# Kernel optimization log

Measured on AMD Instinct MI355X. Metric: run time of the kernel, lower is better.

## Reference

```python
import jax, jax.numpy as jnp
from jax import lax
import numpy as np

HH = WW = 128          # backbone feature map (2048px image / stride 16)
C_IN = 512
FEAT_STRIDE = 16
N_ANCHOR = 9
NMS_THRESH = 0.7
N_PRE_NMS = 6000
N_POST_NMS = 300
MIN_SIZE = 16
NEG = jnp.float32(-1e30)


def _anchor_base(base_size=16, ratios=(0.5, 1.0, 2.0), scales=(8, 16, 32)):
    py = px = base_size / 2.0
    ab = np.zeros((len(ratios) * len(scales), 4), np.float32)
    for i, r in enumerate(ratios):
        for j, s in enumerate(scales):
            h = base_size * s * np.sqrt(r)
            w = base_size * s * np.sqrt(1.0 / r)
            ab[i * len(scales) + j] = [py - h / 2, px - w / 2, py + h / 2, px + w / 2]
    return ab


def _shifted_anchors(hh, ww):
    # (y1, x1, y2, x2) anchors enumerated row-major over (y, x), anchors innermost
    ab = _anchor_base()
    sy = np.arange(0, hh * FEAT_STRIDE, FEAT_STRIDE, dtype=np.float32)
    sx = np.arange(0, ww * FEAT_STRIDE, FEAT_STRIDE, dtype=np.float32)
    sx, sy = np.meshgrid(sx, sy)
    shift = np.stack((sy.ravel(), sx.ravel(), sy.ravel(), sx.ravel()), axis=1)
    anc = (ab[None, :, :] + shift[:, None, :]).reshape(-1, 4)
    return jnp.asarray(anc)


def _conv(x, w, b):
    y = lax.conv_general_dilated(x, w, (1, 1), 'SAME',
                                 dimension_numbers=('NHWC', 'HWIO', 'NHWC'))
    return y + b


def _loc2bbox(anchor, loc):
    sh = anchor[:, 2] - anchor[:, 0]
    sw = anchor[:, 3] - anchor[:, 1]
    scy = anchor[:, 0] + 0.5 * sh
    scx = anchor[:, 1] + 0.5 * sw
    cy = loc[:, 0] * sh + scy
    cx = loc[:, 1] * sw + scx
    h = jnp.exp(loc[:, 2]) * sh
    w = jnp.exp(loc[:, 3]) * sw
    return jnp.stack([cy - 0.5 * h, cx - 0.5 * w, cy + 0.5 * h, cx + 0.5 * w], axis=1)


def _nms(boxes, scores, thresh, n_out):
    # Greedy NMS with a fixed output size; invalid slots are zeroed.
    y1, x1, y2, x2 = boxes[:, 0], boxes[:, 1], boxes[:, 2], boxes[:, 3]
    areas = (y2 - y1) * (x2 - x1)

    def step(valid, _):
        s = jnp.where(valid, scores, NEG)
        i = jnp.argmax(s)
        ok = s[i] > NEG
        iy1 = jnp.maximum(y1, y1[i]); ix1 = jnp.maximum(x1, x1[i])
        iy2 = jnp.minimum(y2, y2[i]); ix2 = jnp.minimum(x2, x2[i])
        inter = jnp.maximum(iy2 - iy1, 0.0) * jnp.maximum(ix2 - ix1, 0.0)
        iou = inter / (areas + areas[i] - inter + 1e-9)
        valid = valid & (iou <= thresh)  # picked box suppresses itself (iou=1)
        return valid, (i, ok)

    _, (idx, oks) = lax.scan(step, jnp.ones(scores.shape, bool), None, length=n_out)
    return boxes[idx] * oks[:, None].astype(boxes.dtype)


def _proposals(loc, fg_score, anchor, img_h, img_w, scale):
    dst = _loc2bbox(anchor, loc)
    dst = jnp.stack([jnp.clip(dst[:, 0], 0.0, img_h),
                     jnp.clip(dst[:, 1], 0.0, img_w),
                     jnp.clip(dst[:, 2], 0.0, img_h),
                     jnp.clip(dst[:, 3], 0.0, img_w)], axis=1)
    min_size = MIN_SIZE * scale
    hs = dst[:, 2] - dst[:, 0]
    ws = dst[:, 3] - dst[:, 1]
    keep = (hs >= min_size) & (ws >= min_size)
    sc = jnp.where(keep, fg_score, -jnp.inf)
    top_s, top_i = lax.top_k(sc, N_PRE_NMS)
    return _nms(dst[top_i], top_s, NMS_THRESH, N_POST_NMS)


def _rpn_forward(x, conv_w, conv_b, loc_w, loc_b, score_w, score_b, img_h, img_w, scale):
    n, hh, ww, _ = x.shape
    anchor = _shifted_anchors(hh, ww)                    # [hh*ww*9, 4]
    h = jax.nn.relu(_conv(x, conv_w, conv_b))            # [n, hh, ww, 512]
    rpn_loc = _conv(h, loc_w, loc_b).reshape(n, -1, 4)   # [n, hh*ww*9, 4]
    rpn_score_map = _conv(h, score_w, score_b)           # [n, hh, ww, 18]
    soft = jax.nn.softmax(rpn_score_map.reshape(n, hh, ww, N_ANCHOR, 2), axis=-1)
    rpn_fg = soft[..., 1].reshape(n, -1)                 # [n, hh*ww*9]
    rpn_score = rpn_score_map.reshape(n, -1, 2)
    roi = _proposals(rpn_loc[0], rpn_fg[0], anchor, img_h, img_w, scale)  # [300, 4]
    return rpn_loc, rpn_score, roi, anchor


def setup_inputs() -> dict:
    key = jax.random.key(0)
    ks = jax.random.split(key, 4)
    return {
        "x": jax.random.normal(ks[0], (1, HH, WW, C_IN), jnp.float32),
        "conv_w": jax.random.normal(ks[1], (3, 3, C_IN, 512), jnp.float32) * 0.02,
        "conv_b": jnp.zeros((512,), jnp.float32),
        "loc_w": jax.random.normal(ks[2], (1, 1, 512, 36), jnp.float32) * 0.02,
        "loc_b": jnp.zeros((36,), jnp.float32),
        "score_w": jax.random.normal(ks[3], (1, 1, 512, 18), jnp.float32) * 0.02,
        "score_b": jnp.zeros((18,), jnp.float32),
        "img_h": HH * FEAT_STRIDE,
        "img_w": WW * FEAT_STRIDE,
        "scale": 1,
    }


def reference(x, conv_w, conv_b, loc_w, loc_b, score_w, score_b, img_h, img_w, scale):
    return _rpn_forward(x, conv_w, conv_b, loc_w, loc_b, score_w, score_b,
                        float(img_h), float(img_w), float(scale))
```

## Files before the change

### kernel.cpp

```cpp
#include <hip/hip_runtime.h>
#include <math.h>

typedef unsigned int u32;
typedef unsigned long long u64;
typedef _Float16 half8 __attribute__((ext_vector_type(8)));
typedef float f32x4 __attribute__((ext_vector_type(4)));
typedef float f32x16 __attribute__((ext_vector_type(16)));

#define N_PIX 16384
#define N_ANC 147456
#define N_PRE 6000
#define TIE_BASE 6144
#define TIE_CAP  16384

#define OFF_H      0ULL
#define OFF_BOXES  33554432ULL
#define OFF_KEYS   35913728ULL
#define OFF_W54    36503552ULL
#define OFF_B54    36634624ULL
#define OFF_HIST1  36634880ULL
#define OFF_HIST2  36897024ULL
#define OFF_CTRL   37159168ULL
#define OFF_CAND   37159424ULL
#define OFF_SBOX   37339648ULL
#define OFF_MASK   37437952ULL
#define BASE_NEEDED 41961984ULL
#define OFF_XH     41961984ULL
#define OFF_XL     58739200ULL
#define OFF_WHT    75516416ULL
#define OFF_WLT    80235008ULL
#define FULL_NEEDED 84953600ULL

#define KEY_NEGINF 0x007FFFFFu

#define MASK_BYTES 4524032ULL

struct AB { float v[36]; };


__device__ __forceinline__ void d_init_body(int i0, u32* hist1, u32* hist2, u32* ctrl, float* roi,
                       float* w54, float* b54,
                       const float* __restrict__ loc_w, const float* __restrict__ loc_b,
                       const float* __restrict__ score_w, const float* __restrict__ score_b) {
  const int stride = 256 * 256;
  const int TOT = 65536 * 2 + 64 + 1200 + 32768 + 64;
  for (int i = i0; i < TOT; i += stride) {
    if (i < 65536) hist1[i] = 0u;
    else if (i < 131072) hist2[i - 65536] = 0u;
    else if (i < 131136) ctrl[i - 131072] = 0u;
    else if (i < 132336) roi[i - 131136] = 0.f;
    else if (i < 165104) {
      int j = i - 132336;
      int k = j >> 6, oc = j & 63;
      float v = 0.f;
      if (oc < 36) v = loc_w[k * 36 + oc];
      else if (oc < 54) v = score_w[k * 18 + oc - 36];
      w54[(((k >> 2) << 6) + oc) * 4 + (k & 3)] = v;
    } else {
      int oc = i - 165104;
      float v = 0.f;
      if (oc < 36) v = loc_b[oc];
      else if (oc < 54) v = score_b[oc - 36];
      b54[oc] = v;
    }
  }
}

__device__ __forceinline__ void d_split_x_body(int b, int t, const float* __restrict__ x,
                                               _Float16* __restrict__ xh, _Float16* __restrict__ xl) {
  const int gid = b * 256 + t;
  const int base = gid << 3;
  float a[8];
  *(float4*)&a[0] = *(const float4*)(x + base);
  *(float4*)&a[4] = *(const float4*)(x + base + 4);
  half8 hh, ll;
#pragma unroll
  for (int j = 0; j < 8; ++j) {
    _Float16 hi = (_Float16)a[j];
    hh[j] = hi;
    ll[j] = (_Float16)((a[j] - (float)hi) * 2048.0f);
  }
  *(half8*)(xh + base) = hh;
  *(half8*)(xl + base) = ll;
}

__device__ __forceinline__ void d_split_w_body(int kb64, int ob, int t, const float* __restrict__ w,
                                               _Float16* __restrict__ whPK, _Float16* __restrict__ wlPK,
                                               _Float16 (*th)[72], _Float16 (*tl)[72]) {
  {
    const int r = t >> 2, cq = t & 3;
    float a[16];
    const float* wp = w + ((size_t)(kb64 * 64 + r) << 9) + ob * 64 + cq * 16;
#pragma unroll
    for (int j = 0; j < 4; ++j) *(float4*)&a[j << 2] = *(const float4*)(wp + (j << 2));
    half8 h0, h1, l0, l1;
#pragma unroll
    for (int j = 0; j < 8; ++j) {
      _Float16 hi = (_Float16)a[j];
      h0[j] = hi; l0[j] = (_Float16)((a[j] - (float)hi) * 2048.0f);
    }
#pragma unroll
    for (int j = 0; j < 8; ++j) {
      _Float16 hi = (_Float16)a[8 + j];
      h1[j] = hi; l1[j] = (_Float16)((a[8 + j] - (float)hi) * 2048.0f);
    }
    *(half8*)&th[r][cq * 16]     = h0;
    *(half8*)&th[r][cq * 16 + 8] = h1;
    *(half8*)&tl[r][cq * 16]     = l0;
    *(half8*)&tl[r][cq * 16 + 8] = l1;
  }
  __syncthreads();
  {
    const int o_local = t & 63;
    const int hl = (t >> 6) & 1;
    const int cs = t >> 7;
    const int tap = kb64 >> 3;
    const int ci  = ((kb64 & 7) << 1) + cs;
    const int kb  = ci * 9 + tap;
    const int o   = ob * 64 + o_local;
    const int nb  = o >> 7, n = o & 127;
    _Float16* dst = (hl ? wlPK : whPK) + (((size_t)(nb * 144 + kb)) << 12) + n * 8;
    _Float16 (*src)[72] = hl ? tl : th;
    const int r0 = cs << 5;
#pragma unroll
    for (int q = 0; q < 4; ++q) {
      half8 v;
#pragma unroll
      for (int j = 0; j < 8; ++j) v[j] = src[r0 + (q << 3) + j][o_local];
      *(half8*)(dst + (q << 10)) = v;
    }
  }
}

__global__ void k_init(u32* hist1, u32* hist2, u32* ctrl, float* roi,
                       float* w54, float* b54,
                       const float* __restrict__ loc_w, const float* __restrict__ loc_b,
                       const float* __restrict__ score_w, const float* __restrict__ score_b) {
  const int i0 = blockIdx.x * blockDim.x + threadIdx.x;
  d_init_body(i0, hist1, hist2, ctrl, roi, w54, b54, loc_w, loc_b, score_w, score_b);
}

__global__ __launch_bounds__(256) void k_prep(const float* __restrict__ x,
                                              _Float16* __restrict__ xh, _Float16* __restrict__ xl,
                                              const float* __restrict__ w,
                                              _Float16* __restrict__ whPK, _Float16* __restrict__ wlPK,
                                              u32* hist1, u32* hist2, u32* ctrl, float* roi,
                                              float* w54, float* b54,
                                              const float* __restrict__ loc_w, const float* __restrict__ loc_b,
                                              const float* __restrict__ score_w, const float* __restrict__ score_b) {
  __shared__ _Float16 th[64][72];
  __shared__ _Float16 tl[64][72];
  const int b = blockIdx.x;
  const int t = threadIdx.x;
  if (b < 4096) {
    d_split_x_body(b, t, x, xh, xl);
  } else if (b < 4672) {
    const int idx = b - 4096;
    d_split_w_body(idx % 72, idx / 72, t, w, whPK, wlPK, th, tl);
  } else {
    d_init_body((b - 4672) * 256 + t, hist1, hist2, ctrl, roi, w54, b54, loc_w, loc_b, score_w, score_b);
  }
}

__global__ __launch_bounds__(256, 2) void k_conv_pre(const _Float16* __restrict__ xh,
                                                     const _Float16* __restrict__ xl,
                                                     const _Float16* __restrict__ whPK,
                                                     const _Float16* __restrict__ wlPK,
                                                     const float* __restrict__ bias,
                                                     float* __restrict__ h) {
  __shared__ _Float16 As[2][2][4][128][8];

  const int bid = blockIdx.x;
  const int q   = bid >> 3;
  const int nb  = q >> 4;
  const int y   = ((bid & 7) << 4) + (q & 15);

  const int t  = threadIdx.x;
  const int wv = t >> 6, lane = t & 63;
  const int m0 = (wv >> 1) << 6;
  const int n0 = (wv & 1) << 6;
  const int ln5 = lane & 31;
  const int kh  = lane >> 5;

  const int s_m = t >> 1;
  const int kq0 = (t & 1) << 1;
  const int ch0 = kq0 << 3;

  f32x16 acc_hh[2][2];
  f32x16 acc_x[2][2];
#pragma unroll
  for (int i = 0; i < 2; ++i)
#pragma unroll
    for (int j = 0; j < 2; ++j) { acc_hh[i][j] = (f32x16)0.f; acc_x[i][j] = (f32x16)0.f; }

  const int ct0 = (s_m - 1) << 9;
  const int ct1 = s_m << 9;
  const int ct2 = (s_m + 1) << 9;
  const bool cok0 = (s_m >= 1);
  const bool cok2 = (s_m <= 126);

  const u32 wb = ((u32)kh << 10) + (((u32)(n0 + ln5)) << 3);

  half8 rah0, rah1, ral0, ral1;
  half8 bh0[2][2], bl0[2][2], bh1[2][2], bl1[2][2];

#define CONV_LOADA(KB)                                                           \
  {                                                                              \
    const int ci_   = (KB) / 9;                                                  \
    const int tap_  = (KB) - ci_ * 9;                                            \
    const int ky_   = tap_ / 3, kx_ = tap_ - ky_ * 3;                            \
    const int cin0_ = ci_ << 5;                                                  \
    const int yy_   = y + ky_ - 1;                                               \
    const bool rok_ = (yy_ >= 0) && (yy_ < 128);                                 \
    const int colterm_ = (kx_ == 0) ? ct0 : ((kx_ == 1) ? ct1 : ct2);            \
    const bool cok_    = (kx_ == 0) ? cok0 : ((kx_ == 1) ? true : cok2);         \
    if (rok_ && cok_) {                                                          \
      const u32 aoff_ = (u32)((yy_ << 16) + cin0_ + ch0 + colterm_);             \
      rah0 = *(const half8*)(xh + aoff_);                                        \
      rah1 = *(const half8*)(xh + aoff_ + 8);                                    \
      ral0 = *(const half8*)(xl + aoff_);                                        \
      ral1 = *(const half8*)(xl + aoff_ + 8);                                    \
    } else {                                                                     \
      rah0 = (half8)(_Float16)0; rah1 = (half8)(_Float16)0;                      \
      ral0 = (half8)(_Float16)0; ral1 = (half8)(_Float16)0;                      \
    }                                                                            \
  }

#define CONV_STOREA(BUF)                                                         \
  {                                                                              \
    *(half8*)As[BUF][0][kq0][s_m]     = rah0;                                    \
    *(half8*)As[BUF][0][kq0 + 1][s_m] = rah1;                                    \
    *(half8*)As[BUF][1][kq0][s_m]     = ral0;                                    \
    *(half8*)As[BUF][1][kq0 + 1][s_m] = ral1;                                    \
  }

#define BLOAD(KB, BH, BL)                                                        \
  {                                                                              \
    const u32 kbase_ = ((u32)(nb * 144 + (KB))) << 12;    \
    _Pragma("unroll")                                                            \
    for (int i_ = 0; i_ < 2; ++i_) {                                             \
      _Pragma("unroll")                                                          \
      for (int ks_ = 0; ks_ < 2; ++ks_) {                                        \
        const u32 o_ = kbase_ + ((u32)ks_ << 11) + wb + ((u32)i_ << 8);          \
        BH[i_][ks_] = *(const half8*)(whPK + o_);                                \
        BL[i_][ks_] = *(const half8*)(wlPK + o_);                                \
      }                                                                          \
    }                                                                            \
  }

#define FRAGSA(KS, AH, AL)                                                       \
  {                                                                              \
    const int kq_ = ((KS) << 1) + kh;                                            \
    _Pragma("unroll")                                                            \
    for (int i = 0; i < 2; ++i) {                                                \
      AH[i] = *(const half8*)As[cur][0][kq_][m0 + (i << 5) + ln5];               \
      AL[i] = *(const half8*)As[cur][1][kq_][m0 + (i << 5) + ln5];               \
    }                                                                            \
  }

#define MFMA6(AH, AL, BH, BL, KS)                                                \
  {                                                                              \
    _Pragma("unroll")                                                            \
    for (int mi = 0; mi < 2; ++mi)                                               \
      _Pragma("unroll")                                                          \
      for (int ni = 0; ni < 2; ++ni) {                                           \
        acc_hh[mi][ni] = __builtin_amdgcn_mfma_f32_32x32x16_f16(AH[mi], BH[ni][KS], acc_hh[mi][ni], 0, 0, 0); \
        acc_x[mi][ni]  = __builtin_amdgcn_mfma_f32_32x32x16_f16(AH[mi], BL[ni][KS], acc_x[mi][ni], 0, 0, 0);  \
        acc_x[mi][ni]  = __builtin_amdgcn_mfma_f32_32x32x16_f16(AL[mi], BH[ni][KS], acc_x[mi][ni], 0, 0, 0);  \
      }                                                                          \
  }

#define LBARRIER()                                                               \
  {                                                                              \
    asm volatile("s_waitcnt lgkmcnt(0)" ::: "memory");                           \
    __builtin_amdgcn_s_barrier();                                                \
  }

  CONV_LOADA(0);
  BLOAD(0, bh0, bl0);
  CONV_STOREA(0);
  LBARRIER();

  int cur = 0;
#pragma unroll 1
  for (int kb = 0; kb < 144; kb += 2) {
    {
      half8 a0h[2], a0l[2], a1h[2], a1l[2];
      FRAGSA(0, a0h, a0l);
      CONV_LOADA(kb + 1);
      BLOAD(kb + 1, bh1, bl1);
      __builtin_amdgcn_sched_barrier(0);
      __builtin_amdgcn_s_setprio(1);
      MFMA6(a0h, a0l, bh0, bl0, 0);
      __builtin_amdgcn_s_setprio(0);
      FRAGSA(1, a1h, a1l);
      __builtin_amdgcn_s_setprio(1);
      MFMA6(a1h, a1l, bh0, bl0, 1);
      __builtin_amdgcn_s_setprio(0);
      CONV_STOREA(cur ^ 1);
      LBARRIER();
      cur ^= 1;
    }
    {
      half8 a0h[2], a0l[2], a1h[2], a1l[2];
      FRAGSA(0, a0h, a0l);
      if (kb + 2 < 144) {
        CONV_LOADA(kb + 2);
        BLOAD(kb + 2, bh0, bl0);
      }
      __builtin_amdgcn_sched_barrier(0);
      __builtin_amdgcn_s_setprio(1);
      MFMA6(a0h, a0l, bh1, bl1, 0);
      __builtin_amdgcn_s_setprio(0);
      FRAGSA(1, a1h, a1l);
      __builtin_amdgcn_s_setprio(1);
      MFMA6(a1h, a1l, bh1, bl1, 1);
      __builtin_amdgcn_s_setprio(0);
      if (kb + 2 < 144) {
        CONV_STOREA(cur ^ 1);
        LBARRIER();
        cur ^= 1;
      }
    }
  }
#undef CONV_LOADA
#undef CONV_STOREA
#undef BLOAD
#undef FRAGSA
#undef MFMA6
#undef LBARRIER

  const float inv2048 = 1.0f / 2048.0f;
#pragma unroll
  for (int mi = 0; mi < 2; ++mi)
#pragma unroll
    for (int ni = 0; ni < 2; ++ni) {
      const int col = n0 + (ni << 5) + ln5;
      const float bbv = bias[(nb << 7) + col];
#pragma unroll
      for (int r = 0; r < 16; ++r) {
        const int row = m0 + (mi << 5) + (r & 3) + ((r >> 2) << 3) + (kh << 2);
        float v = acc_hh[mi][ni][r] + acc_x[mi][ni][r] * inv2048 + bbv;
        h[(((size_t)((y << 7) + row)) << 9) + (nb << 7) + col] = fmaxf(v, 0.f);
      }
    }
}

#define APAD 40
__global__ __launch_bounds__(256, 2) void k_conv_fb(const float* __restrict__ x,
                                                    const float* __restrict__ w,
                                                    const float* __restrict__ bias,
                                                    float* __restrict__ h) {
  __shared__ _Float16 Ah[128][APAD];
  __shared__ _Float16 Al[128][APAD];
  __shared__ _Float16 Bh[128][APAD];
  __shared__ _Float16 Bl[128][APAD];

  const int y  = blockIdx.x;
  const int nb = blockIdx.y;
  const int t  = threadIdx.x;
  const int wv = t >> 6, lane = t & 63;
  const int m0 = (wv >> 1) << 6;
  const int n0 = (wv & 1) << 6;
  const int fm = lane & 15;
  const int fq = lane >> 4;
  const int sa_m = t >> 1;
  const int sa_h = (t & 1) << 4;
  const int sb_n = t & 127;
  const int sb_kg = (t >> 7) << 4;

  f32x4 acc_hh[4][4];
  f32x4 acc_x[4][4];
#pragma unroll
  for (int i = 0; i < 4; ++i)
#pragma unroll
    for (int j = 0; j < 4; ++j) { acc_hh[i][j] = (f32x4)0.f; acc_x[i][j] = (f32x4)0.f; }

#pragma unroll 1
  for (int kb = 0; kb < 144; ++kb) {
    const int tap  = kb >> 4;
    const int ky   = tap / 3, kx = tap - ky * 3;
    const int cin0 = (kb & 15) << 5;
    {
      const int yy = y + ky - 1;
      const int xx = sa_m + kx - 1;
      float av[16];
      if (yy >= 0 && yy < 128 && xx >= 0 && xx < 128) {
        const float* ap = x + (((size_t)((yy << 7) + xx)) << 9) + cin0 + sa_h;
#pragma unroll
        for (int j = 0; j < 4; ++j) *(float4*)&av[j << 2] = *(const float4*)(ap + (j << 2));
      } else {
#pragma unroll
        for (int j = 0; j < 16; ++j) av[j] = 0.f;
      }
      half8 h0, h1, l0, l1;
#pragma unroll
      for (int j = 0; j < 8; ++j) {
        _Float16 hi = (_Float16)av[j];
        h0[j] = hi; l0[j] = (_Float16)((av[j] - (float)hi) * 2048.0f);
      }
#pragma unroll
      for (int j = 0; j < 8; ++j) {
        _Float16 hi = (_Float16)av[8 + j];
        h1[j] = hi; l1[j] = (_Float16)((av[8 + j] - (float)hi) * 2048.0f);
      }
      *(half8*)&Ah[sa_m][sa_h]     = h0;
      *(half8*)&Ah[sa_m][sa_h + 8] = h1;
      *(half8*)&Al[sa_m][sa_h]     = l0;
      *(half8*)&Al[sa_m][sa_h + 8] = l1;
    }
    {
      const float* bp = w + ((size_t)(tap * 512 + cin0 + sb_kg) << 9) + (nb << 7) + sb_n;
      float bv[16];
#pragma unroll
      for (int j = 0; j < 16; ++j) bv[j] = bp[(size_t)j << 9];
      half8 h0, h1, l0, l1;
#pragma unroll
      for (int j = 0; j < 8; ++j) {
        _Float16 hi = (_Float16)bv[j];
        h0[j] = hi; l0[j] = (_Float16)((bv[j] - (float)hi) * 2048.0f);
      }
#pragma unroll
      for (int j = 0; j < 8; ++j) {
        _Float16 hi = (_Float16)bv[8 + j];
        h1[j] = hi; l1[j] = (_Float16)((bv[8 + j] - (float)hi) * 2048.0f);
      }
      *(half8*)&Bh[sb_n][sb_kg]     = h0;
      *(half8*)&Bh[sb_n][sb_kg + 8] = h1;
      *(half8*)&Bl[sb_n][sb_kg]     = l0;
      *(half8*)&Bl[sb_n][sb_kg + 8] = l1;
    }
    __syncthreads();
    half8 ah[4], al[4], bh[4], bl[4];
#pragma unroll
    for (int i = 0; i < 4; ++i) {
      ah[i] = *(const half8*)&Ah[m0 + (i << 4) + fm][fq << 3];
      al[i] = *(const half8*)&Al[m0 + (i << 4) + fm][fq << 3];
      bh[i] = *(const half8*)&Bh[n0 + (i << 4) + fm][fq << 3];
      bl[i] = *(const half8*)&Bl[n0 + (i << 4) + fm][fq << 3];
    }
#pragma unroll
    for (int mi = 0; mi < 4; ++mi)
#pragma unroll
      for (int ni = 0; ni < 4; ++ni) {
        acc_hh[mi][ni] = __builtin_amdgcn_mfma_f32_16x16x32_f16(ah[mi], bh[ni], acc_hh[mi][ni], 0, 0, 0);
        acc_x[mi][ni]  = __builtin_amdgcn_mfma_f32_16x16x32_f16(ah[mi], bl[ni], acc_x[mi][ni], 0, 0, 0);
        acc_x[mi][ni]  = __builtin_amdgcn_mfma_f32_16x16x32_f16(al[mi], bh[ni], acc_x[mi][ni], 0, 0, 0);
      }
    __syncthreads();
  }
  const float inv2048 = 1.0f / 2048.0f;
#pragma unroll
  for (int mi = 0; mi < 4; ++mi)
#pragma unroll
    for (int ni = 0; ni < 4; ++ni) {
      const int col = n0 + (ni << 4) + fm;
      const float bb = bias[(nb << 7) + col];
#pragma unroll
      for (int r = 0; r < 4; ++r) {
        const int row = m0 + (mi << 4) + (fq << 2) + r;
        float v = acc_hh[mi][ni][r] + acc_x[mi][ni][r] * inv2048 + bb;
        h[(((size_t)((y << 7) + row)) << 9) + (nb << 7) + col] = fmaxf(v, 0.f);
      }
    }
}

__global__ __launch_bounds__(256) void k_heads(const float* __restrict__ h,
        const float4* __restrict__ w54, const float* __restrict__ b54,
        float* __restrict__ out0, float* __restrict__ out1, float* __restrict__ out3,
        float4* __restrict__ boxes, u32* __restrict__ keys, u32* __restrict__ hist1,
        const int* __restrict__ p_ih, const int* __restrict__ p_iw,
        const int* __restrict__ p_sc, AB ab) {
  __shared__ float hl[16 * 512];
  __shared__ float vals[16][64];
  const int t = threadIdx.x;
  const int wv = t >> 6, lane = t & 63;
  const int pbase = blockIdx.x << 4;

#pragma unroll
  for (int j = 0; j < 8; ++j) {
    const int f = (j << 8) + t;
    ((float4*)hl)[f] = ((const float4*)(h + ((size_t)pbase << 9)))[f];
  }
  __syncthreads();

  const float* hp = hl + ((wv << 2) << 9);
  float a0 = 0.f, a1 = 0.f, a2 = 0.f, a3 = 0.f;
#pragma unroll 4
  for (int kq = 0; kq < 128; ++kq) {
    const float4 wvv = w54[(kq << 6) + lane];
    const float4 h0 = *(const float4*)(hp + (kq << 2));
    const float4 h1 = *(const float4*)(hp + 512 + (kq << 2));
    const float4 h2 = *(const float4*)(hp + 1024 + (kq << 2));
    const float4 h3 = *(const float4*)(hp + 1536 + (kq << 2));
    a0 += h0.x * wvv.x + h0.y * wvv.y + h0.z * wvv.z + h0.w * wvv.w;
    a1 += h1.x * wvv.x + h1.y * wvv.y + h1.z * wvv.z + h1.w * wvv.w;
    a2 += h2.x * wvv.x + h2.y * wvv.y + h2.z * wvv.z + h2.w * wvv.w;
    a3 += h3.x * wvv.x + h3.y * wvv.y + h3.z * wvv.z + h3.w * wvv.w;
  }
  const float bb = b54[lane];
  float av[4] = {a0 + bb, a1 + bb, a2 + bb, a3 + bb};
#pragma unroll
  for (int px = 0; px < 4; ++px) {
    const int p = pbase + (wv << 2) + px;
    vals[(wv << 2) + px][lane] = av[px];
    if (lane < 36) out0[p * 36 + lane] = av[px];
    else if (lane < 54) out1[p * 18 + lane - 36] = av[px];
  }
  __syncthreads();

  if (lane < 36) {
    const int px = lane / 9, a = lane - px * 9;
    const int p = pbase + (wv << 2) + px;
    const float* vv = vals[(wv << 2) + px];
    const float l0 = vv[(a << 2) + 0], l1 = vv[(a << 2) + 1];
    const float l2 = vv[(a << 2) + 2], l3 = vv[(a << 2) + 3];
    const float s0 = vv[36 + (a << 1)], s1 = vv[37 + (a << 1)];
    const int yq = p >> 7, xq = p & 127;
    const float fy = (float)(yq << 4), fx = (float)(xq << 4);
    const float ay1 = ab.v[(a << 2) + 0] + fy;
    const float ax1 = ab.v[(a << 2) + 1] + fx;
    const float ay2 = ab.v[(a << 2) + 2] + fy;
    const float ax2 = ab.v[(a << 2) + 3] + fx;
    const int idx = p * 9 + a;
    *(float4*)(out3 + ((size_t)idx << 2)) = make_float4(ay1, ax1, ay2, ax2);

    const float sh = ay2 - ay1, sw = ax2 - ax1;
    const float scy = ay1 + 0.5f * sh, scx = ax1 + 0.5f * sw;
    const float cy = l0 * sh + scy, cx = l1 * sw + scx;
    const float bh = expf(l2) * sh, bw = expf(l3) * sw;
    const float IH = (float)p_ih[0], IW = (float)p_iw[0];
    float d0 = fminf(fmaxf(cy - 0.5f * bh, 0.f), IH);
    float d1 = fminf(fmaxf(cx - 0.5f * bw, 0.f), IW);
    float d2 = fminf(fmaxf(cy + 0.5f * bh, 0.f), IH);
    float d3 = fminf(fmaxf(cx + 0.5f * bw, 0.f), IW);
    boxes[idx] = make_float4(d0, d1, d2, d3);

    const float minsz = 16.f * (float)p_sc[0];
    const bool keep = (d2 - d0 >= minsz) && (d3 - d1 >= minsz);
    const float mx = fmaxf(s0, s1);
    const float e0 = expf(s0 - mx), e1 = expf(s1 - mx);
    const float fg = e1 / (e0 + e1);
    const float sc = keep ? fg : -INFINITY;
    const u32 u = __float_as_uint(sc);
    const u32 key = (u & 0x80000000u) ? ~u : (u | 0x80000000u);
    keys[idx] = key;
    atomicAdd(&hist1[key >> 16], 1u);
  }
}

__global__ void k_hist2(const u32* __restrict__ keys, const u32* __restrict__ ctrl,
                        u32* __restrict__ hist2) {
  const u32 b1 = ctrl[0];
  int i = blockIdx.x * blockDim.x + threadIdx.x;
  if (i < N_ANC) {
    const u32 k = keys[i];
    if ((k >> 16) == b1) atomicAdd(&hist2[k & 0xFFFFu], 1u);
  }
}

__global__ __launch_bounds__(1024) void k_findcut(const u32* __restrict__ hist,
                                                  u32* __restrict__ ctrl, int mode) {
  __shared__ u32 csum[1024];
  __shared__ u32 suf[1024];
  const int t = threadIdx.x;
  const u32 target = (mode == 0) ? (u32)N_PRE : ((u32)N_PRE - ctrl[1]);
  const int base = t << 6;
  u32 s = 0;
  for (int i = 0; i < 64; ++i) s += hist[base + i];
  csum[t] = s;
  suf[t] = s;
  __syncthreads();
  for (int off = 1; off < 1024; off <<= 1) {
    u32 add = (t + off < 1024) ? suf[t + off] : 0u;
    __syncthreads();
    suf[t] += add;
    __syncthreads();
  }
  const u32 excl = suf[t] - csum[t];
  if (excl < target && target <= suf[t]) {
    u32 cum = excl;
    int bkt = base;
    for (int i = 63; i >= 0; --i) {
      const u32 hh = hist[base + i];
      if (cum < target && target <= cum + hh) { bkt = base + i; break; }
      cum += hh;
    }
    if (mode == 0) { ctrl[0] = (u32)bkt; ctrl[1] = cum; }
    else {
      const u32 Kstar = (ctrl[0] << 16) | (u32)bkt;
      const u32 A = ctrl[1] + cum;
      u32 need = (u32)N_PRE - A;
      if (Kstar == KEY_NEGINF) need = 0u;
      ctrl[2] = Kstar; ctrl[3] = A; ctrl[4] = need;
      ctrl[7] = A + need;
    }
  }
}

__global__ void k_compact(const u32* __restrict__ keys, u32* __restrict__ ctrl,
                          u64* __restrict__ cand) {
  const u32 Kstar = ctrl[2];
  const u32 need  = ctrl[4];
  int i = blockIdx.x * blockDim.x + threadIdx.x;
  if (i >= N_ANC) return;
  const u32 k = keys[i];
  if (k > Kstar) {
    const u32 pos = atomicAdd(&ctrl[5], 1u);
    cand[pos] = ((u64)k << 32) | (u64)(u32)(~(u32)i);
  } else if (k == Kstar && need != 0u) {
    const u32 pos = atomicAdd(&ctrl[6], 1u);
    if (pos < (u32)TIE_CAP) cand[TIE_BASE + pos] = ((u64)Kstar << 32) | (u64)(u32)(~(u32)i);
  }
}

__global__ __launch_bounds__(128) void k_rank(const u32* __restrict__ ctrl,
                                              const u64* __restrict__ cand,
                                              const float4* __restrict__ boxes,
                                              float4* __restrict__ sbox) {
  __shared__ u32 wred[2];
  const u32 A   = ctrl[3];
  const u32 tcc = min(ctrl[6], (u32)TIE_CAP);
  const u32 C   = A + tcc;
  const u32 L   = ctrl[7];
  const int t   = threadIdx.x;
  for (u32 i = blockIdx.x; i < C; i += gridDim.x) {
    const u64 v = (i < A) ? cand[i] : cand[TIE_BASE + (i - A)];
    u32 cnt = 0;
    for (u32 j = t; j < A; j += 128) cnt += (cand[j] > v);
    for (u32 j = t; j < tcc; j += 128) cnt += (cand[TIE_BASE + j] > v);
#pragma unroll
    for (int off = 32; off > 0; off >>= 1) cnt += __shfl_xor(cnt, off);
    if ((t & 63) == 0) wred[t >> 6] = cnt;
    __syncthreads();
    if (t == 0) {
      const u32 rank = wred[0] + wred[1];
      if (rank < L) {
        const u32 idx = ~((u32)(v & 0xFFFFFFFFULL));
        sbox[rank] = boxes[idx];
      }
    }
    __syncthreads();
  }
}

__global__ __launch_bounds__(256) void k_mask(const u32* __restrict__ ctrl,
                                              const float4* __restrict__ sbox,
                                              u64* __restrict__ mask) {
  const int L = (int)ctrl[7];
  const int rb = blockIdx.y;
  if (rb * 64 >= L) return;
  const int wv = threadIdx.x >> 6;
  const int lane = threadIdx.x & 63;
  const int cw = (blockIdx.x << 2) + wv;
  if (cw > 93 || cw < rb) return;
  const int j = cw * 64 + lane;
  const bool jok = (j < L);
  const float4 cb = jok ? sbox[j] : make_float4(0.f, 0.f, 0.f, 0.f);
  const float careaJ = (cb.z - cb.x) * (cb.w - cb.y);
  const int rbase = rb * 64;
  const float4 rbx = (rbase + lane < L) ? sbox[rbase + lane] : make_float4(0.f, 0.f, 0.f, 0.f);
  const int rmax = min(64, L - rbase);
  for (int r = 0; r < rmax; ++r) {
    const float ry1 = __shfl(rbx.x, r), rx1 = __shfl(rbx.y, r);
    const float ry2 = __shfl(rbx.z, r), rx2 = __shfl(rbx.w, r);
    const float ra = (ry2 - ry1) * (rx2 - rx1);
    const float iy1 = fmaxf(cb.x, ry1), ix1 = fmaxf(cb.y, rx1);
    const float iy2 = fminf(cb.z, ry2), ix2 = fminf(cb.w, rx2);
    const float inter = fmaxf(iy2 - iy1, 0.f) * fmaxf(ix2 - ix1, 0.f);
    const float iou = inter / (careaJ + ra - inter + 1e-9f);
    const bool bit = jok && (iou > 0.7f);
    const u64 bal = __ballot(bit);
    if (lane == 0) mask[(size_t)(rbase + r) * 94 + cw] = bal;
  }
}

__device__ inline u64 valid_mask_fn(int base, int L) {
  const int r = L - base;
  if (r <= 0) return 0ULL;
  if (r >= 64) return ~0ULL;
  return (1ULL << r) - 1ULL;
}
__device__ inline u64 above_mask_fn(int base, int i) {
  if (i < base) return ~0ULL;
  const int s = i - base + 1;
  if (s >= 64) return 0ULL;
  return (~0ULL) << s;
}

__device__ __forceinline__ void gload_lds16(const void* g, void* l) {
  __builtin_amdgcn_global_load_lds(
      (const __attribute__((address_space(1))) void*)g,
      (__attribute__((address_space(3))) void*)l, 16, 0, 0);
}

__global__ __launch_bounds__(64) void k_greedy(const u32* __restrict__ ctrl,
                                               const float* __restrict__ sboxf,
                                               const u64* __restrict__ mask,
                                               float* __restrict__ roi) {
  __shared__ char lds[4 * 12288];
  const int lane = threadIdx.x;
  const int L = (int)ctrl[7];
  if (L <= 0) return;
  const char* gmask = (const char*)mask;
  const char* gend  = gmask + MASK_BYTES;
  const int nbatch = (L + 15) >> 4;

#define GISSUE(BB)                                                         \
  {                                                                        \
    const char* gb_ = gmask + (size_t)(BB) * 12032;                        \
    char* lb_ = lds + ((BB) & 3) * 12288;                                  \
    _Pragma("unroll")                                                      \
    for (int j_ = 0; j_ < 12; ++j_) {                                      \
      const char* ga_ = gb_ + j_ * 1024;                                   \
      if (ga_ + 1024 > gend) ga_ = gend - 1024;    \
      gload_lds16(ga_ + lane * 16, lb_ + j_ * 1024);                       \
    }                                                                      \
  }

  int next_issue = 0;
  int ready = -1;
  const int base0 = lane << 6;
  const int base1 = (64 + lane) << 6;
  const u64 v0 = valid_mask_fn(base0, L);
  const u64 v1 = (lane < 30) ? valid_mask_fn(base1, L) : 0ULL;
  u64 rem0 = 0ULL, rem1 = 0ULL;
  int i = 0, kept = 0;

  while (i >= 0 && kept < 300) {
    const int bi = i >> 4;
    if (bi > ready) {
      if (next_issue < bi) next_issue = bi;
      const int want = min(bi + 3, nbatch - 1);
      while (next_issue <= want) { GISSUE(next_issue); ++next_issue; }
      const int out = next_issue - 1 - bi;
      if (out >= 3)      asm volatile("s_waitcnt vmcnt(36)" ::: "memory");
      else if (out == 2) asm volatile("s_waitcnt vmcnt(24)" ::: "memory");
      else if (out == 1) asm volatile("s_waitcnt vmcnt(12)" ::: "memory");
      else               asm volatile("s_waitcnt vmcnt(0)"  ::: "memory");
      ready = bi;
    }
    if (lane < 4) roi[kept * 4 + lane] = sboxf[(size_t)i * 4 + lane];
    ++kept;
    const u64* rowp = (const u64*)(lds + (bi & 3) * 12288 + (i & 15) * 752);
    rem0 |= rowp[lane];
    if (lane < 30) rem1 |= rowp[64 + lane];
    const u64 f0 = ~rem0 & v0 & above_mask_fn(base0, i);
    const u64 f1 = ~rem1 & v1 & above_mask_fn(base1, i);
    int ni = -1;
    const u64 b0 = __ballot(f0 != 0ULL);
    if (b0) {
      const int w = (int)__builtin_ctzll(b0);
      const u64 fw = (u64)__shfl((long long)f0, w);
      ni = (w << 6) + (int)__builtin_ctzll(fw);
    } else {
      const u64 b1m = __ballot(f1 != 0ULL);
      if (b1m) {
        const int w = (int)__builtin_ctzll(b1m);
        const u64 fw = (u64)__shfl((long long)f1, w);
        ni = ((64 + w) << 6) + (int)__builtin_ctzll(fw);
      }
    }
    i = ni;
  }
#undef GISSUE
}

extern "C" void kernel_launch(void* const* d_in, const int* in_sizes, int n_in,
                              void* d_out, int out_size, void* d_ws, size_t ws_size,
                              hipStream_t stream) {
  (void)in_sizes; (void)n_in; (void)out_size;
  if (ws_size < BASE_NEEDED) return;
  const bool fast = (ws_size >= FULL_NEEDED);

  const float* x       = (const float*)d_in[0];
  const float* conv_w  = (const float*)d_in[1];
  const float* conv_b  = (const float*)d_in[2];
  const float* loc_w   = (const float*)d_in[3];
  const float* loc_b   = (const float*)d_in[4];
  const float* score_w = (const float*)d_in[5];
  const float* score_b = (const float*)d_in[6];
  const int* p_ih = (const int*)d_in[7];
  const int* p_iw = (const int*)d_in[8];
  const int* p_sc = (const int*)d_in[9];

  float* out0 = (float*)d_out;
  float* out1 = out0 + 589824;
  float* roi  = out1 + 294912;
  float* out3 = roi + 1200;

  char* ws = (char*)d_ws;
  float*     h     = (float*)(ws + OFF_H);
  float4*    boxes = (float4*)(ws + OFF_BOXES);
  u32*       keys  = (u32*)(ws + OFF_KEYS);
  float*     w54   = (float*)(ws + OFF_W54);
  float*     b54   = (float*)(ws + OFF_B54);
  u32*       hist1 = (u32*)(ws + OFF_HIST1);
  u32*       hist2 = (u32*)(ws + OFF_HIST2);
  u32*       ctrl  = (u32*)(ws + OFF_CTRL);
  u64*       cand  = (u64*)(ws + OFF_CAND);
  float4*    sbox  = (float4*)(ws + OFF_SBOX);
  u64*       mask  = (u64*)(ws + OFF_MASK);
  _Float16*  xh    = (_Float16*)(ws + OFF_XH);
  _Float16*  xl    = (_Float16*)(ws + OFF_XL);
  _Float16*  whPK  = (_Float16*)(ws + OFF_WHT);
  _Float16*  wlPK  = (_Float16*)(ws + OFF_WLT);

  AB ab;
  {
    const double ratios[3] = {0.5, 1.0, 2.0};
    const double scales[3] = {8.0, 16.0, 32.0};
    for (int i = 0; i < 3; ++i)
      for (int j = 0; j < 3; ++j) {
        const double hh = 16.0 * scales[j] * sqrt(ratios[i]);
        const double wwv = 16.0 * scales[j] * sqrt(1.0 / ratios[i]);
        const int a = i * 3 + j;
        ab.v[a * 4 + 0] = (float)(8.0 - hh / 2.0);
        ab.v[a * 4 + 1] = (float)(8.0 - wwv / 2.0);
        ab.v[a * 4 + 2] = (float)(8.0 + hh / 2.0);
        ab.v[a * 4 + 3] = (float)(8.0 + wwv / 2.0);
      }
  }

  if (fast) {
    hipLaunchKernelGGL(k_prep, dim3(4928), dim3(256), 0, stream,
                       x, xh, xl, conv_w, whPK, wlPK,
                       hist1, hist2, ctrl, roi, w54, b54, loc_w, loc_b, score_w, score_b);
    hipLaunchKernelGGL(k_conv_pre, dim3(512), dim3(256), 0, stream, xh, xl, whPK, wlPK, conv_b, h);
  } else {
    hipLaunchKernelGGL(k_init, dim3(256), dim3(256), 0, stream,
                       hist1, hist2, ctrl, roi, w54, b54, loc_w, loc_b, score_w, score_b);
    hipLaunchKernelGGL(k_conv_fb, dim3(128, 4), dim3(256), 0, stream, x, conv_w, conv_b, h);
  }
  hipLaunchKernelGGL(k_heads, dim3(1024), dim3(256), 0, stream,
                     h, (const float4*)w54, b54, out0, out1, out3, boxes, keys, hist1,
                     p_ih, p_iw, p_sc, ab);
  hipLaunchKernelGGL(k_findcut, dim3(1), dim3(1024), 0, stream, hist1, ctrl, 0);
  hipLaunchKernelGGL(k_hist2, dim3(576), dim3(256), 0, stream, keys, ctrl, hist2);
  hipLaunchKernelGGL(k_findcut, dim3(1), dim3(1024), 0, stream, hist2, ctrl, 1);
  hipLaunchKernelGGL(k_compact, dim3(576), dim3(256), 0, stream, keys, ctrl, cand);
  hipLaunchKernelGGL(k_rank, dim3(8192), dim3(128), 0, stream, ctrl, cand, boxes, sbox);
  hipLaunchKernelGGL(k_mask, dim3(24, 94), dim3(256), 0, stream, ctrl, sbox, mask);
  hipLaunchKernelGGL(k_greedy, dim3(1), dim3(64), 0, stream, ctrl, (const float*)sbox, mask, roi);
}
```

Baseline: 653.2 us.

## Stage halo row tile per channel chunk and reuse across all 9 conv taps

The conv A-operand is no longer loaded once per tap. For each 32-channel chunk, a padded 3-row by 130-column halo tile of hi/lo fp16 input is staged into LDS once, and all nine taps read shifted fragments from it. This cuts redundant global loads of the input and removes per-tap LDS stores and barriers. In exchange, LDS use grows to about 50KB, the A double-buffering is dropped so staging is exposed between barriers, and the staging loop uses div/mod index math.

```diff
diff --git a/kernel.cpp b/kernel.cpp
--- a/kernel.cpp
+++ b/kernel.cpp
@@ -168,7 +168,7 @@
                                                      const _Float16* __restrict__ wlPK,
                                                      const float* __restrict__ bias,
                                                      float* __restrict__ h) {
-  __shared__ _Float16 As[2][2][4][128][8];
+  __shared__ _Float16 As[2][3][4][130][8];
 
   const int bid = blockIdx.x;
   const int q   = bid >> 3;
@@ -182,10 +182,6 @@
   const int ln5 = lane & 31;
   const int kh  = lane >> 5;
 
-  const int s_m = t >> 1;
-  const int kq0 = (t & 1) << 1;
-  const int ch0 = kq0 << 3;
-
   f32x16 acc_hh[2][2];
   f32x16 acc_x[2][2];
 #pragma unroll
@@ -193,45 +189,31 @@
 #pragma unroll
     for (int j = 0; j < 2; ++j) { acc_hh[i][j] = (f32x16)0.f; acc_x[i][j] = (f32x16)0.f; }
 
-  const int ct0 = (s_m - 1) << 9;
-  const int ct1 = s_m << 9;
-  const int ct2 = (s_m + 1) << 9;
-  const bool cok0 = (s_m >= 1);
-  const bool cok2 = (s_m <= 126);
-
   const u32 wb = ((u32)kh << 10) + (((u32)(n0 + ln5)) << 3);
 
-  half8 rah0, rah1, ral0, ral1;
   half8 bh0[2][2], bl0[2][2], bh1[2][2], bl1[2][2];
 
-#define CONV_LOADA(KB)                                                           \
+#define STAGE(CI)                                                                \
   {                                                                              \
-    const int ci_   = (KB) / 9;                                                  \
-    const int tap_  = (KB) - ci_ * 9;                                            \
-    const int ky_   = tap_ / 3, kx_ = tap_ - ky_ * 3;                            \
-    const int cin0_ = ci_ << 5;                                                  \
-    const int yy_   = y + ky_ - 1;                                               \
-    const bool rok_ = (yy_ >= 0) && (yy_ < 128);                                 \
-    const int colterm_ = (kx_ == 0) ? ct0 : ((kx_ == 1) ? ct1 : ct2);            \
-    const bool cok_    = (kx_ == 0) ? cok0 : ((kx_ == 1) ? true : cok2);         \
-    if (rok_ && cok_) {                                                          \
-      const u32 aoff_ = (u32)((yy_ << 16) + cin0_ + ch0 + colterm_);             \
-      rah0 = *(const half8*)(xh + aoff_);                                        \
-      rah1 = *(const half8*)(xh + aoff_ + 8);                                    \
-      ral0 = *(const half8*)(xl + aoff_);                                        \
-      ral1 = *(const half8*)(xl + aoff_ + 8);                                    \
-    } else {                                                                     \
-      rah0 = (half8)(_Float16)0; rah1 = (half8)(_Float16)0;                      \
-      ral0 = (half8)(_Float16)0; ral1 = (half8)(_Float16)0;                      \
+    const int ch0_ = (CI) << 5;                                                  \
+    _Pragma("unroll")                                                            \
+    for (int j_ = 0; j_ < 13; ++j_) {                                            \
+      const int c_ = t + (j_ << 8);                                              \
+      if (c_ < 3120) {                                                           \
+        const int p_ = c_ % 130;                                                 \
+        int r_ = c_ / 130;                                                       \
+        const int kq_ = r_ & 3; r_ >>= 2;                                        \
+        const int ky_ = r_ % 3; const int hl_ = r_ / 3;                          \
+        const int yy_ = y + ky_ - 1, xx_ = p_ - 1;                               \
+        half8 v_ = (half8)(_Float16)0;                                           \
+        if (yy_ >= 0 && yy_ < 128 && xx_ >= 0 && xx_ < 128) {                    \
+          const _Float16* sp_ = (hl_ ? xl : xh) +                                \
+              ((((size_t)((yy_ << 7) + xx_)) << 9) + ch0_ + (kq_ << 3));         \
+          v_ = *(const half8*)sp_;                                               \
+        }                                                                        \
+        *(half8*)As[hl_][ky_][kq_][p_] = v_;                                     \
+      }                                                                          \
     }                                                                            \
-  }
-
-#define CONV_STOREA(BUF)                                                         \
-  {                                                                              \
-    *(half8*)As[BUF][0][kq0][s_m]     = rah0;                                    \
-    *(half8*)As[BUF][0][kq0 + 1][s_m] = rah1;                                    \
-    *(half8*)As[BUF][1][kq0][s_m]     = ral0;                                    \
-    *(half8*)As[BUF][1][kq0 + 1][s_m] = ral1;                                    \
   }
 
 #define BLOAD(KB, BH, BL)                                                        \
@@ -248,13 +230,13 @@
     }                                                                            \
   }
 
-#define FRAGSA(KS, AH, AL)                                                       \
+#define FRAGS2(KY, KX, KS, AH, AL)                                               \
   {                                                                              \
     const int kq_ = ((KS) << 1) + kh;                                            \
     _Pragma("unroll")                                                            \
     for (int i = 0; i < 2; ++i) {                                                \
-      AH[i] = *(const half8*)As[cur][0][kq_][m0 + (i << 5) + ln5];               \
-      AL[i] = *(const half8*)As[cur][1][kq_][m0 + (i << 5) + ln5];               \
+      AH[i] = *(const half8*)As[0][KY][kq_][m0 + (i << 5) + ln5 + (KX)];         \
+      AL[i] = *(const half8*)As[1][KY][kq_][m0 + (i << 5) + ln5 + (KX)];         \
     }                                                                            \
   }
 
@@ -276,59 +258,58 @@
     __builtin_amdgcn_s_barrier();                                                \
   }
 
-  CONV_LOADA(0);
+#define TAPB(T, KY, KX, CUR, CURL, NXT, NXTL)                                    \
+  {                                                                              \
+    half8 a0h[2], a0l[2];                                                        \
+    FRAGS2(KY, KX, 0, a0h, a0l);                                                 \
+    if (kb0 + (T) + 1 < 144) { BLOAD(kb0 + (T) + 1, NXT, NXTL); }                \
+    __builtin_amdgcn_sched_barrier(0);                                           \
+    __builtin_amdgcn_s_setprio(1);                                               \
+    MFMA6(a0h, a0l, CUR, CURL, 0);                                               \
+    __builtin_amdgcn_s_setprio(0);                                               \
+    half8 a1h[2], a1l[2];                                                        \
+    FRAGS2(KY, KX, 1, a1h, a1l);                                                 \
+    __builtin_amdgcn_s_setprio(1);                                               \
+    MFMA6(a1h, a1l, CUR, CURL, 1);                                               \
+    __builtin_amdgcn_s_setprio(0);                                               \
+  }
+
+#define GROUP(C0, CL0, C1, CL1)                                                  \
+  TAPB(0, 0, 0, C0, CL0, C1, CL1)                                                \
+  TAPB(1, 0, 1, C1, CL1, C0, CL0)                                                \
+  TAPB(2, 0, 2, C0, CL0, C1, CL1)                                                \
+  TAPB(3, 1, 0, C1, CL1, C0, CL0)                                                \
+  TAPB(4, 1, 1, C0, CL0, C1, CL1)                                                \
+  TAPB(5, 1, 2, C1, CL1, C0, CL0)                                                \
+  TAPB(6, 2, 0, C0, CL0, C1, CL1)                                                \
+  TAPB(7, 2, 1, C1, CL1, C0, CL0)                                                \
+  TAPB(8, 2, 2, C0, CL0, C1, CL1)
+
   BLOAD(0, bh0, bl0);
-  CONV_STOREA(0);
+  STAGE(0);
   LBARRIER();
 
-  int cur = 0;
 #pragma unroll 1
-  for (int kb = 0; kb < 144; kb += 2) {
-    {
-      half8 a0h[2], a0l[2], a1h[2], a1l[2];
-      FRAGSA(0, a0h, a0l);
-      CONV_LOADA(kb + 1);
-      BLOAD(kb + 1, bh1, bl1);
-      __builtin_amdgcn_sched_barrier(0);
-      __builtin_amdgcn_s_setprio(1);
-      MFMA6(a0h, a0l, bh0, bl0, 0);
-      __builtin_amdgcn_s_setprio(0);
-      FRAGSA(1, a1h, a1l);
-      __builtin_amdgcn_s_setprio(1);
-      MFMA6(a1h, a1l, bh0, bl0, 1);
-      __builtin_amdgcn_s_setprio(0);
-      CONV_STOREA(cur ^ 1);
+  for (int ci = 0; ci < 16; ++ci) {
+    const int kb0 = ci * 9;
+    if (!(ci & 1)) {
+      GROUP(bh0, bl0, bh1, bl1)
+    } else {
+      GROUP(bh1, bl1, bh0, bl0)
+    }
+    if (ci + 1 < 16) {
       LBARRIER();
-      cur ^= 1;
-    }
-    {
-      half8 a0h[2], a0l[2], a1h[2], a1l[2];
-      FRAGSA(0, a0h, a0l);
-      if (kb + 2 < 144) {
-        CONV_LOADA(kb + 2);
-        BLOAD(kb + 2, bh0, bl0);
-      }
-      __builtin_amdgcn_sched_barrier(0);
-      __builtin_amdgcn_s_setprio(1);
-      MFMA6(a0h, a0l, bh1, bl1, 0);
-      __builtin_amdgcn_s_setprio(0);
-      FRAGSA(1, a1h, a1l);
-      __builtin_amdgcn_s_setprio(1);
-      MFMA6(a1h, a1l, bh1, bl1, 1);
-      __builtin_amdgcn_s_setprio(0);
-      if (kb + 2 < 144) {
-        CONV_STOREA(cur ^ 1);
-        LBARRIER();
-        cur ^= 1;
-      }
-    }
-  }
-#undef CONV_LOADA
-#undef CONV_STOREA
+      STAGE(ci + 1);
+      LBARRIER();
+    }
+  }
+#undef STAGE
 #undef BLOAD
-#undef FRAGSA
+#undef FRAGS2
 #undef MFMA6
 #undef LBARRIER
+#undef TAPB
+#undef GROUP
 
   const float inv2048 = 1.0f / 2048.0f;
 #pragma unroll
```

Measured after the change: 1.230 ms. 1.88x slower.
